# Kernel optimization log

Hardware: AMD Instinct MI355X
Metric: run time of the kernel (lower is better)

## Reference

```python
import jax, jax.numpy as jnp
import numpy as np

BATCH, NODE, DIM = 4, 2048, 128
EPS = 1e-5


def _bn(x, gamma, beta):
    # BatchNorm1d in training mode: biased batch stats over rows, per-feature.
    mu = jnp.mean(x, axis=0)
    var = jnp.var(x, axis=0)
    return (x - mu) * jax.lax.rsqrt(var + EPS) * gamma + beta


def setup_inputs() -> dict:
    key = jax.random.key(0)
    ks = jax.random.split(key, 8)
    N = BATCH * NODE
    # Scale L like a normalized graph operator so activations stay sane.
    L = jax.random.normal(ks[0], (N, N), dtype=jnp.float32) / np.sqrt(N)
    inputs = jax.random.normal(ks[1], (BATCH, NODE, DIM), dtype=jnp.float32)
    mask = jnp.zeros((BATCH, NODE, 1), dtype=bool)  # unused in forward
    lim = 1.0 / np.sqrt(2 * DIM)
    fc0_w = jax.random.uniform(ks[2], (DIM, 2 * DIM), jnp.float32, -lim, lim)
    fc0_b = jax.random.uniform(ks[3], (DIM,), jnp.float32, -lim, lim)
    fc1_w = jax.random.uniform(ks[4], (DIM, 2 * DIM), jnp.float32, -lim, lim)
    fc1_b = jax.random.uniform(ks[5], (DIM,), jnp.float32, -lim, lim)
    bn0_gamma = jnp.ones((2 * DIM,), jnp.float32)
    bn0_beta = jnp.zeros((2 * DIM,), jnp.float32)
    bn1_gamma = jnp.ones((2 * DIM,), jnp.float32)
    bn1_beta = jnp.zeros((2 * DIM,), jnp.float32)
    return dict(L=L, mask=mask, inputs=inputs,
                bn0_gamma=bn0_gamma, bn0_beta=bn0_beta, fc0_w=fc0_w, fc0_b=fc0_b,
                bn1_gamma=bn1_gamma, bn1_beta=bn1_beta, fc1_w=fc1_w, fc1_b=fc1_b)


def reference(L, mask, inputs, bn0_gamma, bn0_beta, fc0_w, fc0_b,
              bn1_gamma, bn1_beta, fc1_w, fc1_b):
    b, n, d = inputs.shape

    def block(x, gamma, beta, w, bias):
        # x: (b, n, d). Laplacian propagation over flattened batch*node dim.
        xf = x.reshape(-1, d)                      # (b*n, d)
        Lx = (L @ xf).reshape(b, n, d)
        h = jnp.concatenate([x, Lx], axis=2).reshape(-1, 2 * d)
        h = _bn(h, gamma, beta)                    # pre-BN
        h = h @ w.T + bias                         # Linear(2d -> d)
        return h.reshape(b, n, d)

    x = jax.nn.elu(inputs)
    x = block(x, bn0_gamma, bn0_beta, fc0_w, fc0_b)
    x = jax.nn.elu(x)
    x = block(x, bn1_gamma, bn1_beta, fc1_w, fc1_b)
    return x + inputs
```

## Files before the change

### kernel.cpp

```cpp
#include <hip/hip_runtime.h>
#include <math.h>

#define NROWS 8192
#define DIM   128
#define FEAT  256
#define BK    128
#define NT    (NROWS / BK)

typedef __attribute__((ext_vector_type(8))) __bf16 bf16x8;
typedef __attribute__((ext_vector_type(8))) unsigned short u16x8;
typedef __attribute__((ext_vector_type(4))) unsigned short u16x4;
typedef __attribute__((ext_vector_type(4))) float f32x4;

__device__ __forceinline__ float bf2f(unsigned short h) {
  return __uint_as_float(((unsigned)h) << 16);
}
__device__ __forceinline__ unsigned short f2bf(float f) {
  unsigned u = __float_as_uint(f);
  return (unsigned short)((u + 0x7fff + ((u >> 16) & 1)) >> 16);
}
__device__ __forceinline__ void async16(const void* g, void* l) {
  __builtin_amdgcn_global_load_lds(
      (const __attribute__((address_space(1))) void*)g,
      (__attribute__((address_space(3))) void*)l, 16, 0, 0);
}
__device__ __forceinline__ f32x4 mfma16(bf16x8 a, bf16x8 b, f32x4 c) {
  return __builtin_amdgcn_mfma_f32_16x16x32_bf16(a, b, c, 0, 0, 0);
}
__device__ __forceinline__ float ldp(const void* p, int i, int is32) {
  return is32 ? ((const float*)p)[i] : bf2f(((const unsigned short*)p)[i]);
}

__global__ void detect_kernel(const unsigned short* __restrict__ L,
                              int* __restrict__ flag,
                              float* __restrict__ stats)
{
  for (int i = threadIdx.x; i < 1024; i += 256) stats[i] = 0.f;
  __shared__ int cnt;
  if (threadIdx.x == 0) cnt = 0;
  __syncthreads();
  int c = 0;
  for (int i = 0; i < 16; i++) {
    unsigned short s = L[2 * (threadIdx.x + 256 * i)];
    int e = (s >> 7) & 0xFF;
    if (e >= 192) c++;
  }
  atomicAdd(&cnt, c);
  __syncthreads();
  if (threadIdx.x == 0) *flag = (cnt > 16) ? 1 : 0;
}

__global__ __launch_bounds__(256) void trans_kernel(
    const void* __restrict__ src, unsigned short* __restrict__ xT,
    unsigned short* __restrict__ x0, unsigned short* __restrict__ inpc,
    float* __restrict__ stats, const int* __restrict__ flag)
{
  __shared__ __align__(16) unsigned short T[128 * 136];
  const int tid = threadIdx.x;
  const int r0 = blockIdx.x * 128;
  const int is32 = *flag;
  #pragma unroll
  for (int i = 0; i < 8; i++) {
    const int c = tid + 256 * i;
    const int rr = c >> 4, cg = c & 15;
    const size_t gidx = (size_t)(r0 + rr) * DIM + cg * 8;
    u16x8 v;
    if (is32) {
      const float* s = (const float*)src + gidx;
      f32x4 a = *(const f32x4*)s, b = *(const f32x4*)(s + 4);
      #pragma unroll
      for (int e = 0; e < 4; e++) { v[e] = f2bf(a[e]); v[e + 4] = f2bf(b[e]); }
    } else {
      v = *(const u16x8*)((const unsigned short*)src + gidx);
    }
    *(u16x8*)(inpc + gidx) = v;
    #pragma unroll
    for (int e = 0; e < 8; e++) {
      float f = bf2f(v[e]);
      f = f > 0.f ? f : expm1f(f);
      v[e] = f2bf(f);
    }
    *(u16x8*)(x0 + gidx) = v;
    *(u16x8*)(T + rr * 136 + cg * 8) = v;
  }
  __syncthreads();
  #pragma unroll
  for (int i = 0; i < 8; i++) {
    const int c = tid + 256 * i;
    const int n = c >> 4, mg = c & 15;
    u16x8 v;
    float s = 0.f, q = 0.f;
    #pragma unroll
    for (int e = 0; e < 8; e++) {
      unsigned short h = T[(mg * 8 + e) * 136 + n];
      v[e] = h;
      float f = bf2f(h);
      s += f; q += f * f;
    }
    *(u16x8*)(xT + (size_t)n * NROWS + r0 + mg * 8) = v;
    #pragma unroll
    for (int off = 1; off < 16; off <<= 1) {
      s += __shfl_xor(s, off, 16);
      q += __shfl_xor(q, off, 16);
    }
    if ((tid & 15) == 0) {
      atomicAdd(&stats[n], s);
      atomicAdd(&stats[256 + n], q);
    }
  }
}

template <int IS32>
__device__ __forceinline__ void gemm1_body(
    const void* __restrict__ Lraw, const unsigned short* __restrict__ xT,
    unsigned short* __restrict__ Lxb, float* __restrict__ stats,
    unsigned short* __restrict__ AsBase, unsigned short* __restrict__ BsBase)
{
  const int tid  = threadIdx.x;
  const int lane = tid & 63;
  const int wave = tid >> 6;
  const int kh = wave >> 2, wq = wave & 3;
  const int ln = lane & 15, quad = lane >> 4;
  const int m0 = blockIdx.x * 32;

  const int arow = tid >> 4, ap = tid & 15;
  const int akg = (ap & 8) | ((ap & 7) ^ (arow & 7));
  const float*          Lf = (const float*)Lraw;
  const unsigned short* Lh = (const unsigned short*)Lraw;
  const size_t Abase = (size_t)(m0 + arow) * NROWS + akg * 8;

  int brow[4], bkg[4];
  #pragma unroll
  for (int i = 0; i < 4; i++) {
    const int c = tid + (i << 9);
    brow[i] = c >> 4;
    const int p = c & 15;
    bkg[i] = (p & 8) | ((p & 7) ^ (brow[i] & 7));
  }

  unsigned short* a0 = AsBase;
  unsigned short* a1 = AsBase + 32 * 128;
  unsigned short* a2 = AsBase + 2 * 32 * 128;
  unsigned short* c0 = BsBase;
  unsigned short* c1 = BsBase + 128 * 128;
  unsigned short* c2 = BsBase + 2 * 128 * 128;

  f32x4 acc[2][2];
  #pragma unroll
  for (int i = 0; i < 2; i++)
    #pragma unroll
    for (int j = 0; j < 2; j++)
      acc[i][j] = (f32x4){0.f, 0.f, 0.f, 0.f};

  auto issueB = [&](int kt, unsigned short* Bbuf) {
    const size_t koff = (size_t)kt * BK;
    #pragma unroll
    for (int i = 0; i < 4; i++) {
      const int c = tid + (i << 9);
      async16(xT + (size_t)brow[i] * NROWS + koff + bkg[i] * 8, Bbuf + c * 8);
    }
  };
  auto loadA = [&](int kt, f32x4& r0, f32x4& r1) {
    const float* s = Lf + Abase + (size_t)kt * BK;
    r0 = *(const f32x4*)s;
    r1 = *(const f32x4*)(s + 4);
  };
  auto issueA16 = [&](int kt, unsigned short* Abuf) {
    async16(Lh + Abase + (size_t)kt * BK, Abuf + arow * 128 + ap * 8);
  };
  auto writeA = [&](const f32x4& r0, const f32x4& r1, unsigned short* Abuf) {
    u16x8 o;
    #pragma unroll
    for (int e = 0; e < 4; e++) { o[e] = f2bf(r0[e]); o[e + 4] = f2bf(r1[e]); }
    *(u16x8*)(Abuf + arow * 128 + ap * 8) = o;
  };
  auto compute = [&](const unsigned short* Abuf, const unsigned short* Bbuf) {
    #pragma unroll
    for (int s = 0; s < 2; s++) {
      const int kga = kh * 8 + s * 4 + quad;
      const int sw8 = ((kga & 8) | ((kga & 7) ^ (ln & 7))) * 8;
      bf16x8 af0 = *(const bf16x8*)(Abuf + ln * 128 + sw8);
      bf16x8 af1 = *(const bf16x8*)(Abuf + (16 + ln) * 128 + sw8);
      bf16x8 bf0 = *(const bf16x8*)(Bbuf + (wq * 32 + ln) * 128 + sw8);
      bf16x8 bf1 = *(const bf16x8*)(Bbuf + (wq * 32 + 16 + ln) * 128 + sw8);
      acc[0][0] = mfma16(af0, bf0, acc[0][0]);
      acc[0][1] = mfma16(af0, bf1, acc[0][1]);
      acc[1][0] = mfma16(af1, bf0, acc[1][0]);
      acc[1][1] = mfma16(af1, bf1, acc[1][1]);
    }
  };
  auto waitbar = [&]() {
    if (IS32) asm volatile("s_waitcnt vmcnt(6) lgkmcnt(0)" ::: "memory");
    else      asm volatile("s_waitcnt vmcnt(5) lgkmcnt(0)" ::: "memory");
    __builtin_amdgcn_s_barrier();
  };

  f32x4 e0, e1, o0, o1;

  issueB(0, c0);
  if (IS32) loadA(0, e0, e1); else issueA16(0, a0);
  issueB(1, c1);
  if (IS32) loadA(1, o0, o1); else issueA16(1, a1);
  if (IS32) writeA(e0, e1, a0);
  waitbar();

  for (int p = 0; p < 31; ++p) {
    const int t = 2 * p;
    issueB(t + 2, c2);
    if (IS32) loadA(t + 2, e0, e1); else issueA16(t + 2, a2);
    compute(a0, c0);
    if (IS32) writeA(o0, o1, a1);
    waitbar();
    issueB(t + 3, c0);
    if (IS32) loadA(t + 3, o0, o1); else issueA16(t + 3, a0);
    compute(a1, c1);
    if (IS32) writeA(e0, e1, a2);
    waitbar();
    unsigned short* tB = c2; c2 = c1; c1 = c0; c0 = tB;
    unsigned short* tA = a2; a2 = a1; a1 = a0; a0 = tA;
  }

  compute(a0, c0);
  if (IS32) writeA(o0, o1, a1);
  __syncthreads();
  compute(a1, c1);
  __syncthreads();

  float* E = (float*)AsBase;
  #pragma unroll
  for (int i = 0; i < 2; i++)
    #pragma unroll
    for (int j = 0; j < 2; j++)
      if (kh == 0) {
        #pragma unroll
        for (int r = 0; r < 4; r++)
          E[(i * 16 + quad * 4 + r) * 128 + wq * 32 + j * 16 + ln] =
              acc[i][j][r];
      }
  __syncthreads();
  if (kh == 1) {
    #pragma unroll
    for (int i = 0; i < 2; i++)
      #pragma unroll
      for (int j = 0; j < 2; j++)
        #pragma unroll
        for (int r = 0; r < 4; r++)
          E[(i * 16 + quad * 4 + r) * 128 + wq * 32 + j * 16 + ln] +=
              acc[i][j][r];
  }
  __syncthreads();
  {
    const int row = tid >> 4, cc0 = (tid & 15) * 8;
    u16x8 o;
    #pragma unroll
    for (int e = 0; e < 8; e++) o[e] = f2bf(E[row * 128 + cc0 + e]);
    *(u16x8*)(Lxb + (size_t)(m0 + row) * DIM + cc0) = o;
  }
  if (tid < 128) {
    float s = 0.f, q = 0.f;
    #pragma unroll
    for (int r = 0; r < 32; r++) {
      const float v = E[r * 128 + tid];
      s += v; q += v * v;
    }
    atomicAdd(&stats[128 + tid], s);
    atomicAdd(&stats[384 + tid], q);
  }
}

__global__ __launch_bounds__(512) void gemm1_fused(
    const void* __restrict__ Lraw, const unsigned short* __restrict__ xT,
    unsigned short* __restrict__ Lxb, float* __restrict__ stats,
    const int* __restrict__ flag)
{
  __shared__ __align__(16) unsigned short As[3 * 32 * 128];
  __shared__ __align__(16) unsigned short Bs[3 * 128 * 128];
  if (*flag) gemm1_body<1>(Lraw, xT, Lxb, stats, As, Bs);
  else       gemm1_body<0>(Lraw, xT, Lxb, stats, As, Bs);
}

__global__ void prep_kernel(const float* __restrict__ stats,
                            const void* __restrict__ gamma,
                            const void* __restrict__ beta,
                            const void* __restrict__ w,
                            const void* __restrict__ bias,
                            unsigned short* __restrict__ weff,
                            float* __restrict__ beff,
                            const int* __restrict__ flag)
{
  const int is32 = *flag;
  const int k = blockIdx.x;
  const int j = threadIdx.x;
  const float inv = 1.f / 8192.f;
  float mu = stats[j] * inv;
  float var = fmaxf(stats[256 + j] * inv - mu * mu, 0.f);
  float s = ldp(gamma, j, is32) * rsqrtf(var + 1e-5f);
  float wv = ldp(w, k * FEAT + j, is32);
  weff[(size_t)k * FEAT + j] = f2bf(wv * s);
  float term = (ldp(beta, j, is32) - mu * s) * wv;
  __shared__ float red[256];
  red[j] = term;
  __syncthreads();
  for (int off = 128; off > 0; off >>= 1) {
    if (j < off) red[j] += red[j + off];
    __syncthreads();
  }
  if (j == 0) beff[k] = ldp(bias, k, is32) + red[0];
}

__global__ __launch_bounds__(256) void gemm2_fc(
    const unsigned short* __restrict__ xb,
    const unsigned short* __restrict__ Lxb,
    const unsigned short* __restrict__ weff,
    const float* __restrict__ beff,
    const unsigned short* __restrict__ resid,
    void* __restrict__ outv,
    unsigned short* __restrict__ xTout,
    float* __restrict__ statsOut,
    int mode, const int* __restrict__ flag)
{
  __shared__ __align__(16) unsigned short As[32 * 264];
  const int is32 = *flag;
  const int tid = threadIdx.x;
  const int lane = tid & 63, wave = tid >> 6;
  const int m0 = blockIdx.x * 32;

  #pragma unroll
  for (int i = 0; i < 4; i++) {
    const int c = tid + 256 * i;
    const int mr = c >> 5, ch = c & 31;
    const unsigned short* src =
        (ch < 16) ? (xb  + (size_t)(m0 + mr) * DIM + ch * 8)
                  : (Lxb + (size_t)(m0 + mr) * DIM + (ch - 16) * 8);
    *(u16x8*)(As + mr * 264 + ch * 8) = *(const u16x8*)src;
  }
  __syncthreads();

  const int ln = lane & 15, quad = lane >> 4;
  const int nq = wave * 32;
  f32x4 acc[2][2];
  #pragma unroll
  for (int i = 0; i < 2; i++)
    #pragma unroll
    for (int j = 0; j < 2; j++)
      acc[i][j] = (f32x4){0.f, 0.f, 0.f, 0.f};

  #pragma unroll
  for (int ks = 0; ks < 8; ks++) {
    bf16x8 af[2], bfr[2];
    #pragma unroll
    for (int i = 0; i < 2; i++)
      af[i] = *(const bf16x8*)(As + (i * 16 + ln) * 264 + ks * 32 + quad * 8);
    #pragma unroll
    for (int j = 0; j < 2; j++)
      bfr[j] = *(const bf16x8*)(weff + (size_t)(nq + j * 16 + ln) * FEAT +
                                ks * 32 + quad * 8);
    #pragma unroll
    for (int i = 0; i < 2; i++)
      #pragma unroll
      for (int j = 0; j < 2; j++)
        acc[i][j] = mfma16(af[i], bfr[j], acc[i][j]);
  }

  #pragma unroll
  for (int j = 0; j < 2; j++) {
    const int gn = nq + j * 16 + ln;
    const float bb = beff[gn];
    float s = 0.f, q = 0.f;
    #pragma unroll
    for (int i = 0; i < 2; i++) {
      u16x4 pk;
      #pragma unroll
      for (int r = 0; r < 4; r++) {
        const int gm = m0 + i * 16 + quad * 4 + r;
        float v = acc[i][j][r] + bb;
        const size_t idx = (size_t)gm * DIM + gn;
        if (mode == 0) {
          v = v > 0.f ? v : expm1f(v);
          const unsigned short h = f2bf(v);
          ((unsigned short*)outv)[idx] = h;
          pk[r] = h;
          const float hv = bf2f(h);
          s += hv; q += hv * hv;
        } else {
          v += bf2f(resid[idx]);
          if (is32) ((float*)outv)[idx] = v;
          else      ((unsigned short*)outv)[idx] = f2bf(v);
        }
      }
      if (mode == 0)
        *(u16x4*)(xTout + (size_t)gn * NROWS + m0 + i * 16 + quad * 4) = pk;
    }
    if (mode == 0) {
      s += __shfl_xor(s, 16); q += __shfl_xor(q, 16);
      s += __shfl_xor(s, 32); q += __shfl_xor(q, 32);
      if (quad == 0) {
        atomicAdd(&statsOut[gn], s);
        atomicAdd(&statsOut[256 + gn], q);
      }
    }
  }
}

extern "C" void kernel_launch(void* const* d_in, const int* in_sizes, int n_in,
                              void* d_out, int out_size, void* d_ws, size_t ws_size,
                              hipStream_t stream) {
  const void* Lm   = d_in[0];
  const void* inp  = d_in[2];
  const void* bn0g = d_in[3];
  const void* bn0b = d_in[4];
  const void* fc0w = d_in[5];
  const void* fc0b = d_in[6];
  const void* bn1g = d_in[7];
  const void* bn1b = d_in[8];
  const void* fc1w = d_in[9];
  const void* fc1b = d_in[10];

  char* ws = (char*)d_ws;
  unsigned short* xT   = (unsigned short*)(ws);
  unsigned short* x0   = (unsigned short*)(ws + (2ull << 20));
  unsigned short* Lxb  = (unsigned short*)(ws + (4ull << 20));
  unsigned short* x1   = (unsigned short*)(ws + (6ull << 20));
  unsigned short* inpc = (unsigned short*)(ws + (8ull << 20));
  float*          stats= (float*)         (ws + (10ull << 20));
  int*            flag = (int*)           (ws + (10ull << 20) + 8192);
  float*          beff = (float*)         (ws + (10ull << 20) + 12288);
  unsigned short* weff = (unsigned short*)(ws + (10ull << 20) + 16384);

  detect_kernel<<<1, 256, 0, stream>>>((const unsigned short*)Lm, flag, stats);

  trans_kernel<<<64, 256, 0, stream>>>(inp, xT, x0, inpc, stats, flag);
  gemm1_fused<<<256, 512, 0, stream>>>(Lm, xT, Lxb, stats, flag);
  prep_kernel<<<128, 256, 0, stream>>>(stats, bn0g, bn0b, fc0w, fc0b,
                                       weff, beff, flag);
  gemm2_fc<<<256, 256, 0, stream>>>(x0, Lxb, weff, beff, nullptr, x1,
                                    xT, stats + 512, 0, flag);

  gemm1_fused<<<256, 512, 0, stream>>>(Lm, xT, Lxb, stats + 512, flag);
  prep_kernel<<<128, 256, 0, stream>>>(stats + 512, bn1g, bn1b, fc1w, fc1b,
                                       weff, beff, flag);
  gemm2_fc<<<256, 256, 0, stream>>>(x1, Lxb, weff, beff, inpc, d_out,
                                    nullptr, nullptr, 1, flag);
}
```

Measured before the change: 178.8 us.

## Load fp32 L directly into MFMA fragments, skipping LDS staging for A

```diff
diff --git a/kernel.cpp b/kernel.cpp
--- a/kernel.cpp
+++ b/kernel.cpp
@@ -110,9 +110,140 @@
   }
 }
 
-template <int IS32>
-__device__ __forceinline__ void gemm1_body(
-    const void* __restrict__ Lraw, const unsigned short* __restrict__ xT,
+__device__ __forceinline__ void gemm1_f32_body(
+    const float* __restrict__ Lf, const unsigned short* __restrict__ xT,
+    unsigned short* __restrict__ Lxb, float* __restrict__ stats,
+    unsigned short* __restrict__ BsBase)
+{
+  const int tid  = threadIdx.x;
+  const int lane = tid & 63;
+  const int wave = tid >> 6;
+  const int kq = wave >> 1, nh = wave & 1;
+  const int ln = lane & 15, quad = lane >> 4;
+  const int m0 = blockIdx.x * 32;
+
+  int brow[4], bkg[4];
+  #pragma unroll
+  for (int i = 0; i < 4; i++) {
+    const int c = tid + (i << 9);
+    brow[i] = c >> 4;
+    const int p = c & 15;
+    bkg[i] = (p & 8) | ((p & 7) ^ (brow[i] & 7));
+  }
+
+  unsigned short* c0 = BsBase;
+  unsigned short* c1 = BsBase + 128 * 128;
+  unsigned short* c2 = BsBase + 2 * 128 * 128;
+
+  f32x4 acc[2][4];
+  #pragma unroll
+  for (int i = 0; i < 2; i++)
+    #pragma unroll
+    for (int j = 0; j < 4; j++)
+      acc[i][j] = (f32x4){0.f, 0.f, 0.f, 0.f};
+
+  const size_t Afb = (size_t)(m0 + ln) * NROWS + kq * 32 + quad * 8;
+  f32x4 pA0, pA1, pA2, pA3;
+  bf16x8 afc0, afc1;
+
+  auto issueB = [&](int kt, unsigned short* Bbuf) {
+    const size_t koff = (size_t)kt * BK;
+    #pragma unroll
+    for (int i = 0; i < 4; i++) {
+      const int c = tid + (i << 9);
+      async16(xT + (size_t)brow[i] * NROWS + koff + bkg[i] * 8, Bbuf + c * 8);
+    }
+  };
+  auto issueAF = [&](int kt) {
+    const float* b = Lf + Afb + (size_t)kt * BK;
+    pA0 = *(const f32x4*)b;
+    pA1 = *(const f32x4*)(b + 4);
+    pA2 = *(const f32x4*)(b + (size_t)16 * NROWS);
+    pA3 = *(const f32x4*)(b + (size_t)16 * NROWS + 4);
+  };
+  auto cvtA = [&]() {
+    union { u16x8 u; bf16x8 b; } cv0, cv1;
+    #pragma unroll
+    for (int e = 0; e < 4; e++) {
+      cv0.u[e] = f2bf(pA0[e]); cv0.u[e + 4] = f2bf(pA1[e]);
+      cv1.u[e] = f2bf(pA2[e]); cv1.u[e + 4] = f2bf(pA3[e]);
+    }
+    afc0 = cv0.b; afc1 = cv1.b;
+  };
+  auto compute = [&](const unsigned short* Bbuf) {
+    const int kga = kq * 4 + quad;
+    #pragma unroll
+    for (int j = 0; j < 4; j++) {
+      const int nr = nh * 64 + j * 16 + ln;
+      bf16x8 bf = *(const bf16x8*)(Bbuf + nr * 128 +
+                     ((kga & 8) | ((kga & 7) ^ (nr & 7))) * 8);
+      acc[0][j] = mfma16(afc0, bf, acc[0][j]);
+      acc[1][j] = mfma16(afc1, bf, acc[1][j]);
+    }
+  };
+
+  issueAF(0);
+  issueB(0, c0);
+  issueB(1, c1);
+  asm volatile("s_waitcnt vmcnt(4) lgkmcnt(0)" ::: "memory");
+  cvtA();
+  __builtin_amdgcn_s_barrier();
+
+  for (int t = 0; t < 62; ++t) {
+    issueAF(t + 1);
+    issueB(t + 2, c2);
+    compute(c0);
+    asm volatile("s_waitcnt vmcnt(4) lgkmcnt(0)" ::: "memory");
+    cvtA();
+    __builtin_amdgcn_s_barrier();
+    unsigned short* tb = c0; c0 = c1; c1 = c2; c2 = tb;
+  }
+
+  issueAF(63);
+  compute(c0);
+  asm volatile("s_waitcnt vmcnt(4) lgkmcnt(0)" ::: "memory");
+  cvtA();
+  __builtin_amdgcn_s_barrier();
+  compute(c1);
+  __syncthreads();
+
+  float* E = (float*)BsBase;
+  for (int g = 0; g < 4; g++) {
+    if (kq == g) {
+      #pragma unroll
+      for (int i = 0; i < 2; i++)
+        #pragma unroll
+        for (int j = 0; j < 4; j++)
+          #pragma unroll
+          for (int r = 0; r < 4; r++) {
+            float* p = &E[(i * 16 + quad * 4 + r) * 128 + nh * 64 + j * 16 + ln];
+            if (g == 0) *p = acc[i][j][r];
+            else        *p += acc[i][j][r];
+          }
+    }
+    __syncthreads();
+  }
+  {
+    const int row = tid >> 4, cc0 = (tid & 15) * 8;
+    u16x8 o;
+    #pragma unroll
+    for (int e = 0; e < 8; e++) o[e] = f2bf(E[row * 128 + cc0 + e]);
+    *(u16x8*)(Lxb + (size_t)(m0 + row) * DIM + cc0) = o;
+  }
+  if (tid < 128) {
+    float s = 0.f, q = 0.f;
+    #pragma unroll
+    for (int r = 0; r < 32; r++) {
+      const float v = E[r * 128 + tid];
+      s += v; q += v * v;
+    }
+    atomicAdd(&stats[128 + tid], s);
+    atomicAdd(&stats[384 + tid], q);
+  }
+}
+
+__device__ __forceinline__ void gemm1_bf16_body(
+    const unsigned short* __restrict__ Lh, const unsigned short* __restrict__ xT,
     unsigned short* __restrict__ Lxb, float* __restrict__ stats,
     unsigned short* __restrict__ AsBase, unsigned short* __restrict__ BsBase)
 {
@@ -125,8 +256,6 @@
 
   const int arow = tid >> 4, ap = tid & 15;
   const int akg = (ap & 8) | ((ap & 7) ^ (arow & 7));
-  const float*          Lf = (const float*)Lraw;
-  const unsigned short* Lh = (const unsigned short*)Lraw;
   const size_t Abase = (size_t)(m0 + arow) * NROWS + akg * 8;
 
   int brow[4], bkg[4];
@@ -160,19 +289,8 @@
       async16(xT + (size_t)brow[i] * NROWS + koff + bkg[i] * 8, Bbuf + c * 8);
     }
   };
-  auto loadA = [&](int kt, f32x4& r0, f32x4& r1) {
-    const float* s = Lf + Abase + (size_t)kt * BK;
-    r0 = *(const f32x4*)s;
-    r1 = *(const f32x4*)(s + 4);
-  };
   auto issueA16 = [&](int kt, unsigned short* Abuf) {
     async16(Lh + Abase + (size_t)kt * BK, Abuf + arow * 128 + ap * 8);
-  };
-  auto writeA = [&](const f32x4& r0, const f32x4& r1, unsigned short* Abuf) {
-    u16x8 o;
-    #pragma unroll
-    for (int e = 0; e < 4; e++) { o[e] = f2bf(r0[e]); o[e + 4] = f2bf(r1[e]); }
-    *(u16x8*)(Abuf + arow * 128 + ap * 8) = o;
   };
   auto compute = [&](const unsigned short* Abuf, const unsigned short* Bbuf) {
     #pragma unroll
@@ -190,53 +308,41 @@
     }
   };
   auto waitbar = [&]() {
-    if (IS32) asm volatile("s_waitcnt vmcnt(6) lgkmcnt(0)" ::: "memory");
-    else      asm volatile("s_waitcnt vmcnt(5) lgkmcnt(0)" ::: "memory");
+    asm volatile("s_waitcnt vmcnt(5) lgkmcnt(0)" ::: "memory");
     __builtin_amdgcn_s_barrier();
   };
 
-  f32x4 e0, e1, o0, o1;
-
-  issueB(0, c0);
-  if (IS32) loadA(0, e0, e1); else issueA16(0, a0);
-  issueB(1, c1);
-  if (IS32) loadA(1, o0, o1); else issueA16(1, a1);
-  if (IS32) writeA(e0, e1, a0);
+  issueB(0, c0); issueA16(0, a0);
+  issueB(1, c1); issueA16(1, a1);
   waitbar();
 
   for (int p = 0; p < 31; ++p) {
     const int t = 2 * p;
-    issueB(t + 2, c2);
-    if (IS32) loadA(t + 2, e0, e1); else issueA16(t + 2, a2);
+    issueB(t + 2, c2); issueA16(t + 2, a2);
     compute(a0, c0);
-    if (IS32) writeA(o0, o1, a1);
     waitbar();
-    issueB(t + 3, c0);
-    if (IS32) loadA(t + 3, o0, o1); else issueA16(t + 3, a0);
+    issueB(t + 3, c0); issueA16(t + 3, a0);
     compute(a1, c1);
-    if (IS32) writeA(e0, e1, a2);
     waitbar();
     unsigned short* tB = c2; c2 = c1; c1 = c0; c0 = tB;
     unsigned short* tA = a2; a2 = a1; a1 = a0; a0 = tA;
   }
-
   compute(a0, c0);
-  if (IS32) writeA(o0, o1, a1);
   __syncthreads();
   compute(a1, c1);
   __syncthreads();
 
   float* E = (float*)AsBase;
-  #pragma unroll
-  for (int i = 0; i < 2; i++)
-    #pragma unroll
-    for (int j = 0; j < 2; j++)
-      if (kh == 0) {
+  if (kh == 0) {
+    #pragma unroll
+    for (int i = 0; i < 2; i++)
+      #pragma unroll
+      for (int j = 0; j < 2; j++)
         #pragma unroll
         for (int r = 0; r < 4; r++)
           E[(i * 16 + quad * 4 + r) * 128 + wq * 32 + j * 16 + ln] =
               acc[i][j][r];
-      }
+  }
   __syncthreads();
   if (kh == 1) {
     #pragma unroll
@@ -275,8 +381,9 @@
 {
   __shared__ __align__(16) unsigned short As[3 * 32 * 128];
   __shared__ __align__(16) unsigned short Bs[3 * 128 * 128];
-  if (*flag) gemm1_body<1>(Lraw, xT, Lxb, stats, As, Bs);
-  else       gemm1_body<0>(Lraw, xT, Lxb, stats, As, Bs);
+  if (*flag) gemm1_f32_body((const float*)Lraw, xT, Lxb, stats, Bs);
+  else       gemm1_bf16_body((const unsigned short*)Lraw, xT, Lxb, stats,
+                             As, Bs);
 }
 
 __global__ void prep_kernel(const float* __restrict__ stats,
```

Result: slower. 270.3 us (+51.2%).
